# Kernel optimization log

Hardware: AMD Instinct MI355X
Metric: run time of the kernel (lower is better)

Reference implementation:

```python
import jax, jax.numpy as jnp
import numpy as np

B, S1, T = 32, 128, 50
E, H, L, V = 768, 1024, 3, 32000


def setup_inputs() -> dict:
    key = jax.random.key(0)
    ks = jax.random.split(key, 32)
    s = 0.02
    inp = {
        "x": jax.random.normal(ks[0], (B, S1, E), jnp.float32),
        "target_seq": jax.random.randint(ks[1], (B, T), 0, V),
        "emb": jax.random.normal(ks[2], (V, E), jnp.float32) * s,
        "attn_W1": jax.random.normal(ks[3], (H, E + H), jnp.float32) * s,
        "attn_b1": jnp.zeros((H,), jnp.float32),
        "attn_W2": jax.random.normal(ks[4], (1, H), jnp.float32) * s,
        "attn_b2": jnp.zeros((1,), jnp.float32),
        "fc_W": jax.random.normal(ks[5], (V, H), jnp.float32) * s,
        "fc_b": jnp.zeros((V,), jnp.float32),
    }
    for l in range(L):
        in_dim = 2 * E if l == 0 else H
        inp[f"Wih{l}"] = jax.random.normal(ks[6 + 4 * l], (4 * H, in_dim), jnp.float32) * s
        inp[f"Whh{l}"] = jax.random.normal(ks[7 + 4 * l], (4 * H, H), jnp.float32) * s
        inp[f"bih{l}"] = jnp.zeros((4 * H,), jnp.float32)
        inp[f"bhh{l}"] = jnp.zeros((4 * H,), jnp.float32)
    return inp


def _forward(x, target_seq, emb, attn_W1, attn_b1, attn_W2, attn_b2,
             Wih0, Whh0, bih0, bhh0, Wih1, Whh1, bih1, bhh1,
             Wih2, Whh2, bih2, bhh2, fc_W, fc_b):
    Bb, S, Edim = x.shape
    Hd = Whh0.shape[1]
    W1x, W1h = attn_W1[:, :Edim], attn_W1[:, Edim:]
    # precompute encoder-side part of the additive attention MLP: (B, S, H)
    xW = jnp.einsum('bse,he->bsh', x, W1x)
    emb_in = emb[target_seq]  # teacher forcing inputs (B, T, E)
    Wihs = (Wih0, Wih1, Wih2)
    Whhs = (Whh0, Whh1, Whh2)
    bihs = (bih0, bih1, bih2)
    bhhs = (bhh0, bhh1, bhh2)

    def step(carry, cur_in):
        h, c = carry  # each (L, B, H)
        hid = jax.nn.relu(xW + (h[-1] @ W1h.T)[:, None, :] + attn_b1)  # (B,S,H)
        scores = hid @ attn_W2[0] + attn_b2[0]  # (B, S)
        # NOTE: original module multiplies LOG-softmax weights by x (faithful)
        logw = jax.nn.log_softmax(scores, axis=1)[:, :, None]
        context = jnp.sum(logw * x, axis=1)  # (B, E)
        inp = jnp.concatenate([cur_in, context], axis=1)  # (B, 2E)
        new_h, new_c = [], []
        for l in range(3):
            gates = inp @ Wihs[l].T + h[l] @ Whhs[l].T + bihs[l] + bhhs[l]
            i, f, g, o = jnp.split(gates, 4, axis=1)  # torch gate order i,f,g,o
            cl = jax.nn.sigmoid(f) * c[l] + jax.nn.sigmoid(i) * jnp.tanh(g)
            hl = jax.nn.sigmoid(o) * jnp.tanh(cl)
            new_h.append(hl)
            new_c.append(cl)
            inp = hl
        h = jnp.stack(new_h)
        c = jnp.stack(new_c)
        logits = inp @ fc_W.T + fc_b  # (B, V)
        return (h, c), jax.nn.log_softmax(logits, axis=1)

    h0 = jnp.zeros((3, Bb, Hd), x.dtype)
    c0 = jnp.zeros_like(h0)
    _, outs = jax.lax.scan(step, (h0, c0), jnp.swapaxes(emb_in, 0, 1))
    return jnp.swapaxes(outs, 0, 1)  # (B, T, V)


def reference(x, target_seq, emb, attn_W1, attn_b1, attn_W2, attn_b2,
              Wih0, Whh0, bih0, bhh0, Wih1, Whh1, bih1, bhh1,
              Wih2, Whh2, bih2, bhh2, fc_W, fc_b):
    return _forward(x, target_seq, emb, attn_W1, attn_b1, attn_W2, attn_b2,
                    Wih0, Whh0, bih0, bhh0, Wih1, Whh1, bih1, bhh1,
                    Wih2, Whh2, bih2, bhh2, fc_W, fc_b)
```

## Files before the change

### kernel.cpp

```cpp
#include <hip/hip_runtime.h>
#include <math.h>

#define Bdim 32
#define Sdim 128
#define Tdim 50
#define Edim 768
#define Hdim 1024
#define Vdim 32000
#define EH   1792
#define INPD 1536
#define FCB  500

typedef __bf16 bf16x8 __attribute__((ext_vector_type(8)));
typedef float  f32x4  __attribute__((ext_vector_type(4)));

__device__ __forceinline__ float sigmf(float v){ return 1.0f / (1.0f + expf(-v)); }

__device__ __forceinline__ ushort f2b(float v){
  unsigned int b = __float_as_uint(v);
  unsigned int r = (b + 0x7fffu + ((b >> 16) & 1u)) >> 16;
  return (ushort)r;
}
__device__ __forceinline__ float b2f(ushort u){
  return __uint_as_float(((unsigned int)u) << 16);
}

__global__ __launch_bounds__(256) void cvt_bf16(const float* __restrict__ src,
                                                ushort* __restrict__ dst, int n4){
  int i = blockIdx.x * 256 + threadIdx.x;
  if (i >= n4) return;
  float4 v = *(const float4*)(src + (size_t)i * 4);
  *(ushort4*)(dst + (size_t)i * 4) = make_ushort4(f2b(v.x), f2b(v.y), f2b(v.z), f2b(v.w));
}

__global__ __launch_bounds__(256) void cvt_w1h(const float* __restrict__ aW1,
                                               ushort* __restrict__ dst){
  int i = blockIdx.x * 256 + threadIdx.x;
  if (i >= 262144) return;
  int k = (i & 255) * 4;
  int j = i >> 8;
  float4 v = *(const float4*)(aW1 + (size_t)j * EH + Edim + k);
  *(ushort4*)(dst + (size_t)j * 1024 + k) = make_ushort4(f2b(v.x), f2b(v.y), f2b(v.z), f2b(v.w));
}

__global__ __launch_bounds__(256) void zero_kernel(float* __restrict__ p, int n){
  int i = blockIdx.x * 256 + threadIdx.x;
  if (i < n) p[i] = 0.0f;
}

__global__ __launch_bounds__(256) void gather_emb_p(const int* __restrict__ tseq,
                                                    const float* __restrict__ emb,
                                                    ushort* __restrict__ inpP){
  int g = blockIdx.x * 256 + threadIdx.x;
  if (g >= Tdim * Bdim * 96) return;
  int kb = g % 96;
  int r = g / 96;
  int b = r % Bdim;
  int t = r / Bdim;
  int tok = tseq[b * Tdim + t];
  const float* src = emb + (size_t)tok * Edim + kb * 8;
  float4 a = *(const float4*)src;
  float4 c = *(const float4*)(src + 4);
  ushort* dst = inpP + (size_t)t * 49152 + kb * 256 + b * 8;
  *(ushort4*)(dst)     = make_ushort4(f2b(a.x), f2b(a.y), f2b(a.z), f2b(a.w));
  *(ushort4*)(dst + 4) = make_ushort4(f2b(c.x), f2b(c.y), f2b(c.z), f2b(c.w));
}

__global__ __launch_bounds__(256) void xw_gemm(const float* __restrict__ x,
                                               const float* __restrict__ w1,
                                               ushort* __restrict__ xWb){
  __shared__ float As[16][68];
  __shared__ float Ws[16][68];
  int tid = threadIdx.x;
  int m0 = blockIdx.x * 64;
  int n0 = blockIdx.y * 64;
  int lm = tid >> 2;
  int lk = (tid & 3) << 2;
  int tm = (tid >> 4) << 2;
  int tn = (tid & 15) << 2;
  float acc[4][4] = {};
  for (int k0 = 0; k0 < Edim; k0 += 16){
    float4 av = *(const float4*)&x [(size_t)(m0 + lm) * Edim + k0 + lk];
    float4 wv = *(const float4*)&w1[(size_t)(n0 + lm) * EH   + k0 + lk];
    As[lk+0][lm] = av.x; As[lk+1][lm] = av.y; As[lk+2][lm] = av.z; As[lk+3][lm] = av.w;
    Ws[lk+0][lm] = wv.x; Ws[lk+1][lm] = wv.y; Ws[lk+2][lm] = wv.z; Ws[lk+3][lm] = wv.w;
    __syncthreads();
#pragma unroll
    for (int k = 0; k < 16; k++){
      float a0 = As[k][tm+0], a1 = As[k][tm+1], a2 = As[k][tm+2], a3 = As[k][tm+3];
      float b0 = Ws[k][tn+0], b1 = Ws[k][tn+1], b2 = Ws[k][tn+2], b3 = Ws[k][tn+3];
      acc[0][0] += a0*b0; acc[0][1] += a0*b1; acc[0][2] += a0*b2; acc[0][3] += a0*b3;
      acc[1][0] += a1*b0; acc[1][1] += a1*b1; acc[1][2] += a1*b2; acc[1][3] += a1*b3;
      acc[2][0] += a2*b0; acc[2][1] += a2*b1; acc[2][2] += a2*b2; acc[2][3] += a2*b3;
      acc[3][0] += a3*b0; acc[3][1] += a3*b1; acc[3][2] += a3*b2; acc[3][3] += a3*b3;
    }
    __syncthreads();
  }
#pragma unroll
  for (int i = 0; i < 4; i++)
#pragma unroll
    for (int j = 0; j < 4; j++)
      xWb[(size_t)(m0 + tm + i) * Hdim + n0 + tn + j] = f2b(acc[i][j]);
}

template<bool ABF16>
__device__ __forceinline__ void mfma_tile(const void* A, int lda, int r,
                                          const ushort* __restrict__ Bp,
                                          int kbeg, int klen, int lane,
                                          f32x4& acc0, f32x4& acc1){
  int q = lane >> 4;
  const ushort* Ab = (const ushort*)A;
  const float*  Af = (const float*)A;
#pragma unroll 4
  for (int kk = kbeg; kk < kbeg + klen; kk += 32){
    bf16x8 a;
    if (ABF16){
      a = *reinterpret_cast<const bf16x8*>(Ab + (size_t)r * lda + kk + q * 8);
    } else {
      const float* p = Af + (size_t)r * lda + kk + q * 8;
      float4 u = *(const float4*)p;
      float4 w = *(const float4*)(p + 4);
      union { ushort s[8]; bf16x8 v; } t;
      t.s[0]=f2b(u.x); t.s[1]=f2b(u.y); t.s[2]=f2b(u.z); t.s[3]=f2b(u.w);
      t.s[4]=f2b(w.x); t.s[5]=f2b(w.y); t.s[6]=f2b(w.z); t.s[7]=f2b(w.w);
      a = t.v;
    }
    const ushort* bbase = Bp + ((kk >> 3) + q) * 256 + (lane & 15) * 8;
    bf16x8 b0 = *reinterpret_cast<const bf16x8*>(bbase);
    bf16x8 b1 = *reinterpret_cast<const bf16x8*>(bbase + 128);
    acc0 = __builtin_amdgcn_mfma_f32_16x16x32_bf16(a, b0, acc0, 0, 0, 0);
    acc1 = __builtin_amdgcn_mfma_f32_16x16x32_bf16(a, b1, acc1, 0, 0, 0);
  }
}

template<bool ABF16>
__global__ __launch_bounds__(256) void lstm_layer(const void* __restrict__ Wih, int Kin,
                                                  const void* __restrict__ Whh,
                                                  const ushort* __restrict__ inpP,
                                                  const ushort* __restrict__ hP,
                                                  const float* __restrict__ bih,
                                                  const float* __restrict__ bhh,
                                                  const float* __restrict__ cold,
                                                  float* __restrict__ cnew,
                                                  ushort* __restrict__ hPack){
  __shared__ float ld[4][4][4][32];
  int tid = threadIdx.x;
  int lane = tid & 63, kq = tid >> 6;
  int j0 = blockIdx.x * 4;
  int r = ((lane & 15) >> 2) * 1024 + j0 + (lane & 3);
  f32x4 acc0 = {0,0,0,0}, acc1 = {0,0,0,0};
  int kin_q = Kin >> 2;
  mfma_tile<ABF16>(Wih, Kin, r, inpP, kq * kin_q, kin_q, lane, acc0, acc1);
  mfma_tile<ABF16>(Whh, Hdim, r, hP, kq * 256, 256, lane, acc0, acc1);
  int g = lane >> 4, c = lane & 15;
#pragma unroll
  for (int rr = 0; rr < 4; rr++){
    ld[kq][g][rr][c]      = acc0[rr];
    ld[kq][g][rr][c + 16] = acc1[rr];
  }
  __syncthreads();
  if (tid < 128){
    int b = tid & 31, ul = tid >> 5;
    int j = j0 + ul;
    float gi = 0, gf = 0, gg = 0, go = 0;
#pragma unroll
    for (int k = 0; k < 4; k++){
      gi += ld[k][0][ul][b];
      gf += ld[k][1][ul][b];
      gg += ld[k][2][ul][b];
      go += ld[k][3][ul][b];
    }
    gi += bih[j]        + bhh[j];
    gf += bih[j + 1024] + bhh[j + 1024];
    gg += bih[j + 2048] + bhh[j + 2048];
    go += bih[j + 3072] + bhh[j + 3072];
    float cv = sigmf(gf) * cold[j * 32 + b] + sigmf(gi) * tanhf(gg);
    float hv = sigmf(go) * tanhf(cv);
    cnew[j * 32 + b] = cv;
    hPack[(j >> 3) * 256 + b * 8 + (j & 7)] = f2b(hv);
  }
}

__global__ __launch_bounds__(256) void attn_a_gemm(const ushort* __restrict__ W1h,
                                                   const ushort* __restrict__ h2P,
                                                   const float* __restrict__ b1,
                                                   float* __restrict__ aBuf){
  __shared__ float ld[4][32][17];
  int tid = threadIdx.x;
  int lane = tid & 63, kq = tid >> 6;
  int rowBase = blockIdx.x * 16;
  int r = rowBase + (lane & 15);
  f32x4 acc0 = {0,0,0,0}, acc1 = {0,0,0,0};
  mfma_tile<true>(W1h, Hdim, r, h2P, kq * 256, 256, lane, acc0, acc1);
  int q = lane >> 4, c = lane & 15;
#pragma unroll
  for (int rr = 0; rr < 4; rr++){
    ld[kq][c][q * 4 + rr]      = acc0[rr];
    ld[kq][c + 16][q * 4 + rr] = acc1[rr];
  }
  __syncthreads();
  int b = tid & 31, jl = tid >> 5;
#pragma unroll
  for (int h = 0; h < 2; h++){
    int j2 = jl + h * 8;
    float v = ld[0][b][j2] + ld[1][b][j2] + ld[2][b][j2] + ld[3][b][j2];
    int j = rowBase + j2;
    aBuf[b * 1024 + j] = v + b1[j];
  }
}

__global__ __launch_bounds__(256) void attn_score(const float* __restrict__ aBuf,
                                                  const float* __restrict__ w2,
                                                  const float* __restrict__ b2p,
                                                  const ushort* __restrict__ xWb,
                                                  float* __restrict__ scBuf){
  int b = blockIdx.x >> 2, sg = blockIdx.x & 3;
  int w = threadIdx.x >> 6, lane = threadIdx.x & 63;
  int jb = lane * 16;
  float ab[16], wv[16];
#pragma unroll
  for (int i = 0; i < 4; i++){
    *(float4*)&ab[i * 4] = *(const float4*)&aBuf[b * 1024 + jb + i * 4];
    *(float4*)&wv[i * 4] = *(const float4*)&w2[jb + i * 4];
  }
  float b2v = b2p[0];
#pragma unroll
  for (int si = 0; si < 8; si++){
    int s = sg * 32 + w * 8 + si;
    const ushort* xrow = xWb + (size_t)(b * Sdim + s) * Hdim + jb;
    bf16x8 x0 = *reinterpret_cast<const bf16x8*>(xrow);
    bf16x8 x1 = *reinterpret_cast<const bf16x8*>(xrow + 8);
    float acc = 0.0f;
#pragma unroll
    for (int i = 0; i < 8; i++){
      float h0 = fmaxf((float)x0[i] + ab[i], 0.0f);
      float h1 = fmaxf((float)x1[i] + ab[i + 8], 0.0f);
      acc += h0 * wv[i] + h1 * wv[i + 8];
    }
    for (int off = 32; off; off >>= 1) acc += __shfl_xor(acc, off);
    if (lane == 0) scBuf[b * Sdim + s] = acc + b2v;
  }
}

__global__ __launch_bounds__(256) void attn_ctx2(const float* __restrict__ scBuf,
                                                 const ushort* __restrict__ xbf,
                                                 ushort* __restrict__ inpPt){
  __shared__ float sb[Sdim];
  int b = blockIdx.x / 3, ec = blockIdx.x % 3;
  int tid = threadIdx.x;
  if (tid < Sdim) sb[tid] = scBuf[b * Sdim + tid];
  __syncthreads();
  if (tid < 64){
    float v0 = sb[tid], v1 = sb[tid + 64];
    float m = fmaxf(v0, v1);
    for (int off = 32; off; off >>= 1) m = fmaxf(m, __shfl_xor(m, off));
    float e = expf(v0 - m) + expf(v1 - m);
    for (int off = 32; off; off >>= 1) e += __shfl_xor(e, off);
    float lse = m + logf(e);
    sb[tid]      = v0 - lse;
    sb[tid + 64] = v1 - lse;
  }
  __syncthreads();
  int e = ec * 256 + tid;
  const ushort* xb = xbf + (size_t)b * Sdim * Edim + e;
  float acc = 0.0f;
#pragma unroll 8
  for (int s = 0; s < Sdim; s++) acc += sb[s] * b2f(xb[(size_t)s * Edim]);
  int k = Edim + e;
  inpPt[(k >> 3) * 256 + b * 8 + (k & 7)] = f2b(acc);
}

template<bool ABF16>
__global__ __launch_bounds__(512) void fc_gemm(const void* __restrict__ fcW,
                                               const ushort* __restrict__ hP,
                                               const float* __restrict__ fcb,
                                               float* __restrict__ logits,
                                               float* __restrict__ partM,
                                               float* __restrict__ partS){
  __shared__ float ld[2][32][73];
  int tid = threadIdx.x;
  int lane = tid & 63, w = tid >> 6;
  int khalf = w >> 2;
  int v0 = blockIdx.x * 64 + (w & 3) * 16;
  int r = v0 + (lane & 15);
  f32x4 acc0 = {0,0,0,0}, acc1 = {0,0,0,0};
  mfma_tile<ABF16>(fcW, Hdim, r, hP, khalf * 512, 512, lane, acc0, acc1);
  int q = lane >> 4, c = lane & 15;
#pragma unroll
  for (int rr = 0; rr < 4; rr++){
    int vloc = (w & 3) * 16 + q * 4 + rr;
    ld[khalf][c][vloc]      = acc0[rr];
    ld[khalf][c + 16][vloc] = acc1[rr];
  }
  __syncthreads();
  int b = tid >> 4, i0 = (tid & 15) * 4;
  int vg = blockIdx.x * 64 + i0;
  float o0 = ld[0][b][i0+0] + ld[1][b][i0+0] + fcb[vg+0];
  float o1 = ld[0][b][i0+1] + ld[1][b][i0+1] + fcb[vg+1];
  float o2 = ld[0][b][i0+2] + ld[1][b][i0+2] + fcb[vg+2];
  float o3 = ld[0][b][i0+3] + ld[1][b][i0+3] + fcb[vg+3];
  *(float4*)&logits[(size_t)b * Vdim + vg] = make_float4(o0, o1, o2, o3);
  float m = fmaxf(fmaxf(o0, o1), fmaxf(o2, o3));
  float s = expf(o0 - m) + expf(o1 - m) + expf(o2 - m) + expf(o3 - m);
#pragma unroll
  for (int off = 1; off < 16; off <<= 1){
    float m2 = __shfl_xor(m, off);
    float s2 = __shfl_xor(s, off);
    float nm = fmaxf(m, m2);
    s = s * expf(m - nm) + s2 * expf(m2 - nm);
    m = nm;
  }
  if ((tid & 15) == 0){
    partM[b * FCB + blockIdx.x] = m;
    partS[b * FCB + blockIdx.x] = s;
  }
}

__global__ __launch_bounds__(256) void lsm_write(const float* __restrict__ logits,
                                                 const float* __restrict__ partM,
                                                 const float* __restrict__ partS,
                                                 float* __restrict__ out, int t){
  __shared__ float sm[256], ss[256];
  int b = blockIdx.x, chunk = blockIdx.y;
  int tid = threadIdx.x;
  float m = -1e30f, s = 0.0f;
  for (int i = tid; i < FCB; i += 256){
    float m2 = partM[b * FCB + i];
    float s2 = partS[b * FCB + i];
    float nm = fmaxf(m, m2);
    s = s * expf(m - nm) + s2 * expf(m2 - nm);
    m = nm;
  }
  sm[tid] = m; ss[tid] = s;
  __syncthreads();
  for (int r = 128; r; r >>= 1){
    if (tid < r){
      float m2 = sm[tid + r], s2 = ss[tid + r];
      float nm = fmaxf(sm[tid], m2);
      ss[tid] = ss[tid] * expf(sm[tid] - nm) + s2 * expf(m2 - nm);
      sm[tid] = nm;
    }
    __syncthreads();
  }
  float lse = sm[0] + logf(ss[0]);
  if (tid < 250){
    int i4 = chunk * 250 + tid;
    float4 v = ((const float4*)logits)[(size_t)b * 8000 + i4];
    float4* dst = (float4*)(out + ((size_t)b * Tdim + t) * Vdim);
    dst[i4] = make_float4(v.x - lse, v.y - lse, v.z - lse, v.w - lse);
  }
}

extern "C" void kernel_launch(void* const* d_in, const int* in_sizes, int n_in,
                              void* d_out, int out_size, void* d_ws, size_t ws_size,
                              hipStream_t stream){
  const float* x    = (const float*)d_in[0];
  const int*   tseq = (const int*)  d_in[1];
  const float* emb  = (const float*)d_in[2];
  const float* aW1  = (const float*)d_in[3];
  const float* ab1  = (const float*)d_in[4];
  const float* aW2  = (const float*)d_in[5];
  const float* ab2  = (const float*)d_in[6];
  const float* fcW  = (const float*)d_in[7];
  const float* fcb  = (const float*)d_in[8];
  const float* Wih[3] = {(const float*)d_in[9],  (const float*)d_in[13], (const float*)d_in[17]};
  const float* Whh[3] = {(const float*)d_in[10], (const float*)d_in[14], (const float*)d_in[18]};
  const float* bih[3] = {(const float*)d_in[11], (const float*)d_in[15], (const float*)d_in[19]};
  const float* bhh[3] = {(const float*)d_in[12], (const float*)d_in[16], (const float*)d_in[20]};
  float* out = (float*)d_out;

  char* p = (char*)d_ws;
  ushort* xW_bf  = (ushort*)p;            p += (size_t)4096 * 1024 * 2;
  ushort* W1h_bf = (ushort*)p;            p += (size_t)1024 * 1024 * 2;
  ushort* inpP   = (ushort*)p;            p += (size_t)Tdim * 49152 * 2;
  ushort* x_bf   = (ushort*)p;            p += (size_t)Bdim * Sdim * Edim * 2;
  float*  aBuf   = (float*)p;             p += (size_t)Bdim * Hdim * 4;
  float*  scBuf  = (float*)p;             p += (size_t)Bdim * Sdim * 4;
  float*  partM  = (float*)p;             p += (size_t)Bdim * FCB * 4;
  float*  partS  = (float*)p;             p += (size_t)Bdim * FCB * 4;
  float*  logits = (float*)p;             p += (size_t)Bdim * Vdim * 4;
  float*  cBuf   = (float*)p;             p += (size_t)6 * 32768 * 4;
  ushort* hPackB = (ushort*)p;            p += (size_t)6 * 32768 * 2;
  ushort* fcW_bf  = (ushort*)p;           p += (size_t)Vdim * Hdim * 2;
  ushort* Wih_bf[3]; ushort* Whh_bf[3];
  Wih_bf[0] = (ushort*)p;                 p += (size_t)4096 * 1536 * 2;
  Whh_bf[0] = (ushort*)p;                 p += (size_t)4096 * 1024 * 2;
  Wih_bf[1] = (ushort*)p;                 p += (size_t)4096 * 1024 * 2;
  Whh_bf[1] = (ushort*)p;                 p += (size_t)4096 * 1024 * 2;
  Wih_bf[2] = (ushort*)p;                 p += (size_t)4096 * 1024 * 2;
  Whh_bf[2] = (ushort*)p;                 p += (size_t)4096 * 1024 * 2;
  size_t need_full = (size_t)(p - (char*)d_ws);
  bool full = ws_size >= need_full;

  zero_kernel<<<(294912 + 255) / 256, 256, 0, stream>>>(cBuf, 294912);
  gather_emb_p<<<(Tdim * Bdim * 96 + 255) / 256, 256, 0, stream>>>(tseq, emb, inpP);
  cvt_w1h<<<262144 / 256, 256, 0, stream>>>(aW1, W1h_bf);
  cvt_bf16<<<(Bdim * Sdim * Edim / 4 + 255) / 256, 256, 0, stream>>>(x, x_bf, Bdim * Sdim * Edim / 4);
  xw_gemm<<<dim3(64, 16), 256, 0, stream>>>(x, aW1, xW_bf);
  if (full){
    cvt_bf16<<<(Vdim * Hdim / 4 + 255) / 256, 256, 0, stream>>>(fcW, fcW_bf, Vdim * Hdim / 4);
    cvt_bf16<<<(4096 * 1536 / 4 + 255) / 256, 256, 0, stream>>>(Wih[0], Wih_bf[0], 4096 * 1536 / 4);
    cvt_bf16<<<(4096 * 1024 / 4 + 255) / 256, 256, 0, stream>>>(Whh[0], Whh_bf[0], 4096 * 1024 / 4);
    cvt_bf16<<<(4096 * 1024 / 4 + 255) / 256, 256, 0, stream>>>(Wih[1], Wih_bf[1], 4096 * 1024 / 4);
    cvt_bf16<<<(4096 * 1024 / 4 + 255) / 256, 256, 0, stream>>>(Whh[1], Whh_bf[1], 4096 * 1024 / 4);
    cvt_bf16<<<(4096 * 1024 / 4 + 255) / 256, 256, 0, stream>>>(Wih[2], Wih_bf[2], 4096 * 1024 / 4);
    cvt_bf16<<<(4096 * 1024 / 4 + 255) / 256, 256, 0, stream>>>(Whh[2], Whh_bf[2], 4096 * 1024 / 4);
  }

  #define HP(l, par)  (hPackB + ((l) * 2 + (par)) * 32768)
  #define CB(l, par)  (cBuf   + ((l) * 2 + (par)) * 32768)

  for (int t = 0; t < Tdim; t++){
    int pn = t & 1, po = 1 - pn;
    ushort* inpPt = inpP + (size_t)t * 49152;

    attn_a_gemm<<<64, 256, 0, stream>>>(W1h_bf, HP(2, po), ab1, aBuf);
    attn_score<<<128, 256, 0, stream>>>(aBuf, aW2, ab2, xW_bf, scBuf);
    attn_ctx2<<<96, 256, 0, stream>>>(scBuf, x_bf, inpPt);

    for (int l = 0; l < 3; l++){
      const ushort* bin = (l == 0) ? inpPt : HP(l - 1, pn);
      int kin = (l == 0) ? INPD : Hdim;
      if (full)
        lstm_layer<true ><<<256, 256, 0, stream>>>(Wih_bf[l], kin, Whh_bf[l], bin, HP(l, po),
                                                   bih[l], bhh[l], CB(l, po), CB(l, pn), HP(l, pn));
      else
        lstm_layer<false><<<256, 256, 0, stream>>>(Wih[l],    kin, Whh[l],    bin, HP(l, po),
                                                   bih[l], bhh[l], CB(l, po), CB(l, pn), HP(l, pn));
    }

    if (full) fc_gemm<true ><<<FCB, 512, 0, stream>>>(fcW_bf, HP(2, pn), fcb, logits, partM, partS);
    else      fc_gemm<false><<<FCB, 512, 0, stream>>>(fcW,    HP(2, pn), fcb, logits, partM, partS);
    lsm_write<<<dim3(Bdim, 32), 256, 0, stream>>>(logits, partM, partS, out, t);
  }
}
```

Before: 4.001 ms.

## Fuse all decoder timesteps into one persistent kernel with grid barriers

```diff
diff --git a/kernel.cpp b/kernel.cpp
--- a/kernel.cpp
+++ b/kernel.cpp
@@ -10,6 +10,8 @@
 #define EH   1792
 #define INPD 1536
 #define FCB  500
+#define FCB2 250
+#define NBLK 256
 
 typedef __bf16 bf16x8 __attribute__((ext_vector_type(8)));
 typedef float  f32x4  __attribute__((ext_vector_type(4)));
@@ -101,6 +103,28 @@
 #pragma unroll
     for (int j = 0; j < 4; j++)
       xWb[(size_t)(m0 + tm + i) * Hdim + n0 + tn + j] = f2b(acc[i][j]);
+}
+
+__global__ __launch_bounds__(256) void xpose_x(const ushort* __restrict__ xbf,
+                                               ushort* __restrict__ xT){
+  __shared__ ushort tl[64][132];
+  int b  = blockIdx.x / 12;
+  int et = blockIdx.x % 12;
+  int e0 = et * 64;
+  int el = threadIdx.x & 63;
+  int s4 = threadIdx.x >> 6;
+#pragma unroll
+  for (int s0 = 0; s0 < Sdim; s0 += 4){
+    int s = s0 + s4;
+    tl[el][s] = xbf[((size_t)(b * Sdim + s)) * Edim + e0 + el];
+  }
+  __syncthreads();
+  int e  = threadIdx.x >> 2;
+  int sc = (threadIdx.x & 3) * 32;
+  ushort* dst = xT + ((size_t)b * Edim + e0 + e) * Sdim + sc;
+#pragma unroll
+  for (int i = 0; i < 4; i++)
+    *(ushort4*)(dst + i * 8) = *(ushort4*)&tl[e][sc + i * 8];
 }
 
 template<bool ABF16>
@@ -351,6 +375,275 @@
   }
 }
 
+struct PArgs {
+  const ushort *W1h, *xW, *xT, *fcWb;
+  const ushort *Wih0, *Whh0, *Wih1, *Whh1, *Wih2, *Whh2;
+  ushort *inpP, *hPackB;
+  const float *ab1, *aW2, *ab2, *fcb;
+  const float *bih0, *bhh0, *bih1, *bhh1, *bih2, *bhh2;
+  float *aBuf, *partM, *partS, *logits, *cBuf, *out;
+  unsigned *bar;
+};
+
+union ShU {
+  float a8[8][32][17];
+  float sb[Sdim];
+  float ll[8][4][4][32];
+  float fc[32][132];
+  struct { float sm[512]; float ss[512]; } g;
+};
+
+__device__ __forceinline__ void gridbar(unsigned* bar){
+  __syncthreads();
+  if (threadIdx.x == 0){
+    __threadfence();
+    unsigned* gp = bar + 576;
+    unsigned g = __hip_atomic_load(gp, __ATOMIC_RELAXED, __HIP_MEMORY_SCOPE_AGENT);
+    unsigned* cnt = bar + (blockIdx.x & 7) * 64;
+    unsigned a = __hip_atomic_fetch_add(cnt, 1u, __ATOMIC_RELAXED, __HIP_MEMORY_SCOPE_AGENT);
+    if (a == 31u){
+      __hip_atomic_store(cnt, 0u, __ATOMIC_RELAXED, __HIP_MEMORY_SCOPE_AGENT);
+      __threadfence();
+      unsigned r = __hip_atomic_fetch_add(bar + 512, 1u, __ATOMIC_RELAXED, __HIP_MEMORY_SCOPE_AGENT);
+      if (r == 7u){
+        __hip_atomic_store(bar + 512, 0u, __ATOMIC_RELAXED, __HIP_MEMORY_SCOPE_AGENT);
+        __threadfence();
+        __hip_atomic_store(gp, g + 1u, __ATOMIC_RELAXED, __HIP_MEMORY_SCOPE_AGENT);
+      }
+    }
+    int guard = 0;
+    while (__hip_atomic_load(gp, __ATOMIC_RELAXED, __HIP_MEMORY_SCOPE_AGENT) == g){
+      __builtin_amdgcn_s_sleep(2);
+      if (++guard > 300000) break;
+    }
+    __threadfence();
+  }
+  __syncthreads();
+}
+
+__device__ __forceinline__ void lstm_stage(ShU& sh, const ushort* Wih, int Kin,
+                                           const ushort* Whh, const ushort* bin,
+                                           const ushort* hOld,
+                                           const float* bihL, const float* bhhL,
+                                           const float* cOld, float* cNew,
+                                           ushort* hNew, int tid, int lane, int wid,
+                                           int blk){
+  int j0 = blk * 4;
+  int r = ((lane & 15) >> 2) * 1024 + j0 + (lane & 3);
+  f32x4 acc0 = {0,0,0,0}, acc1 = {0,0,0,0};
+  int ke = Kin >> 3;
+  mfma_tile<true>(Wih, Kin, r, bin, wid * ke, ke, lane, acc0, acc1);
+  mfma_tile<true>(Whh, Hdim, r, hOld, wid * 128, 128, lane, acc0, acc1);
+  int g = lane >> 4, c = lane & 15;
+#pragma unroll
+  for (int rr = 0; rr < 4; rr++){
+    sh.ll[wid][g][rr][c]      = acc0[rr];
+    sh.ll[wid][g][rr][c + 16] = acc1[rr];
+  }
+  __syncthreads();
+  if (tid < 128){
+    int b = tid & 31, ul = tid >> 5;
+    int j = j0 + ul;
+    float gi = 0, gf = 0, gg = 0, go = 0;
+#pragma unroll
+    for (int k = 0; k < 8; k++){
+      gi += sh.ll[k][0][ul][b];
+      gf += sh.ll[k][1][ul][b];
+      gg += sh.ll[k][2][ul][b];
+      go += sh.ll[k][3][ul][b];
+    }
+    gi += bihL[j]        + bhhL[j];
+    gf += bihL[j + 1024] + bhhL[j + 1024];
+    gg += bihL[j + 2048] + bhhL[j + 2048];
+    go += bihL[j + 3072] + bhhL[j + 3072];
+    float cv = sigmf(gf) * cOld[j * 32 + b] + sigmf(gi) * tanhf(gg);
+    float hv = sigmf(go) * tanhf(cv);
+    cNew[j * 32 + b] = cv;
+    hNew[(j >> 3) * 256 + b * 8 + (j & 7)] = f2b(hv);
+  }
+}
+
+__global__ __launch_bounds__(512, 2) void persistent_all(PArgs p){
+  extern __shared__ char smem[];
+  ShU& sh = *reinterpret_cast<ShU*>(smem);
+  int tid  = threadIdx.x;
+  int blk  = blockIdx.x;
+  int lane = tid & 63;
+  int wid  = tid >> 6;
+
+  for (int t = 0; t < Tdim; t++){
+    int pn = t & 1, po = 1 - pn;
+    ushort* inpPt = p.inpP + (size_t)t * 49152;
+    const ushort* h2old = p.hPackB + (size_t)(2 * 2 + po) * 32768;
+
+    if (blk < 64){
+      int rowBase = blk * 16;
+      int r = rowBase + (lane & 15);
+      f32x4 acc0 = {0,0,0,0}, acc1 = {0,0,0,0};
+      mfma_tile<true>(p.W1h, Hdim, r, h2old, wid * 128, 128, lane, acc0, acc1);
+      int q = lane >> 4, c = lane & 15;
+#pragma unroll
+      for (int rr = 0; rr < 4; rr++){
+        sh.a8[wid][c][q * 4 + rr]      = acc0[rr];
+        sh.a8[wid][c + 16][q * 4 + rr] = acc1[rr];
+      }
+      __syncthreads();
+      int b = tid & 31, jl = tid >> 5;
+      float v = 0;
+#pragma unroll
+      for (int k = 0; k < 8; k++) v += sh.a8[k][b][jl];
+      int j = rowBase + jl;
+      p.aBuf[b * 1024 + j] = v + p.ab1[j];
+    }
+    gridbar(p.bar);
+
+    if (blk < 32){
+      int b = blk;
+      int jb = lane * 16;
+      float ab[16], w2r[16];
+#pragma unroll
+      for (int i = 0; i < 4; i++){
+        *(float4*)&ab[i * 4]  = *(const float4*)&p.aBuf[b * 1024 + jb + i * 4];
+        *(float4*)&w2r[i * 4] = *(const float4*)&p.aW2[jb + i * 4];
+      }
+      float b2v = p.ab2[0];
+#pragma unroll 2
+      for (int si = 0; si < 16; si++){
+        int s = wid * 16 + si;
+        const ushort* xrow = p.xW + (size_t)(b * Sdim + s) * Hdim + jb;
+        bf16x8 x0 = *reinterpret_cast<const bf16x8*>(xrow);
+        bf16x8 x1 = *reinterpret_cast<const bf16x8*>(xrow + 8);
+        float acc = 0.0f;
+#pragma unroll
+        for (int i = 0; i < 8; i++){
+          float h0 = fmaxf((float)x0[i] + ab[i], 0.0f);
+          float h1 = fmaxf((float)x1[i] + ab[i + 8], 0.0f);
+          acc += h0 * w2r[i] + h1 * w2r[i + 8];
+        }
+        for (int off = 32; off; off >>= 1) acc += __shfl_xor(acc, off);
+        if (lane == 0) sh.sb[s] = acc + b2v;
+      }
+      __syncthreads();
+      if (tid < 64){
+        float v0 = sh.sb[tid], v1 = sh.sb[tid + 64];
+        float m = fmaxf(v0, v1);
+        for (int off = 32; off; off >>= 1) m = fmaxf(m, __shfl_xor(m, off));
+        float e = expf(v0 - m) + expf(v1 - m);
+        for (int off = 32; off; off >>= 1) e += __shfl_xor(e, off);
+        float lse = m + logf(e);
+        sh.sb[tid]      = v0 - lse;
+        sh.sb[tid + 64] = v1 - lse;
+      }
+      __syncthreads();
+#pragma unroll
+      for (int half = 0; half < 2; half++){
+        int e = half * 512 + tid;
+        if (e < Edim){
+          const ushort* xr = p.xT + ((size_t)b * Edim + e) * Sdim;
+          float acc = 0.0f;
+#pragma unroll
+          for (int s8 = 0; s8 < 16; s8++){
+            bf16x8 xv = *reinterpret_cast<const bf16x8*>(xr + s8 * 8);
+#pragma unroll
+            for (int k = 0; k < 8; k++) acc += sh.sb[s8 * 8 + k] * (float)xv[k];
+          }
+          int kk = Edim + e;
+          inpPt[(kk >> 3) * 256 + b * 8 + (kk & 7)] = f2b(acc);
+        }
+      }
+    }
+    gridbar(p.bar);
+
+    {
+      ushort* hb = p.hPackB;  float* cb = p.cBuf;
+      lstm_stage(sh, p.Wih0, INPD, p.Whh0, inpPt,
+                 hb + (0 * 2 + po) * 32768, p.bih0, p.bhh0,
+                 cb + (0 * 2 + po) * 32768, cb + (0 * 2 + pn) * 32768,
+                 hb + (0 * 2 + pn) * 32768, tid, lane, wid, blk);
+      gridbar(p.bar);
+      lstm_stage(sh, p.Wih1, Hdim, p.Whh1, hb + (0 * 2 + pn) * 32768,
+                 hb + (1 * 2 + po) * 32768, p.bih1, p.bhh1,
+                 cb + (1 * 2 + po) * 32768, cb + (1 * 2 + pn) * 32768,
+                 hb + (1 * 2 + pn) * 32768, tid, lane, wid, blk);
+      gridbar(p.bar);
+      lstm_stage(sh, p.Wih2, Hdim, p.Whh2, hb + (1 * 2 + pn) * 32768,
+                 hb + (2 * 2 + po) * 32768, p.bih2, p.bhh2,
+                 cb + (2 * 2 + po) * 32768, cb + (2 * 2 + pn) * 32768,
+                 hb + (2 * 2 + pn) * 32768, tid, lane, wid, blk);
+      gridbar(p.bar);
+    }
+
+    if (blk < FCB2){
+      const ushort* h2new = p.hPackB + (size_t)(2 * 2 + pn) * 32768;
+      int v0 = blk * 128 + wid * 16;
+      int r = v0 + (lane & 15);
+      f32x4 acc0 = {0,0,0,0}, acc1 = {0,0,0,0};
+      mfma_tile<true>(p.fcWb, Hdim, r, h2new, 0, Hdim, lane, acc0, acc1);
+      int q = lane >> 4, c = lane & 15;
+#pragma unroll
+      for (int rr = 0; rr < 4; rr++){
+        sh.fc[c][wid * 16 + q * 4 + rr]      = acc0[rr];
+        sh.fc[c + 16][wid * 16 + q * 4 + rr] = acc1[rr];
+      }
+      __syncthreads();
+      int b = tid >> 4, i0 = (tid & 15) * 8;
+      int vg = blk * 128 + i0;
+      float o[8];
+#pragma unroll
+      for (int j = 0; j < 8; j++) o[j] = sh.fc[b][i0 + j] + p.fcb[vg + j];
+      *(float4*)&p.logits[(size_t)b * Vdim + vg]     = make_float4(o[0], o[1], o[2], o[3]);
+      *(float4*)&p.logits[(size_t)b * Vdim + vg + 4] = make_float4(o[4], o[5], o[6], o[7]);
+      float m = o[0];
+#pragma unroll
+      for (int j = 1; j < 8; j++) m = fmaxf(m, o[j]);
+      float s = 0.0f;
+#pragma unroll
+      for (int j = 0; j < 8; j++) s += expf(o[j] - m);
+#pragma unroll
+      for (int off = 1; off < 16; off <<= 1){
+        float m2 = __shfl_xor(m, off);
+        float s2 = __shfl_xor(s, off);
+        float nm = fmaxf(m, m2);
+        s = s * expf(m - nm) + s2 * expf(m2 - nm);
+        m = nm;
+      }
+      if ((tid & 15) == 0){
+        p.partM[b * FCB2 + blk] = m;
+        p.partS[b * FCB2 + blk] = s;
+      }
+    }
+    gridbar(p.bar);
+
+    {
+      int b = blk >> 3, chunk = blk & 7;
+      float m = -1e30f, s = 0.0f;
+      if (tid < FCB2){ m = p.partM[b * FCB2 + tid]; s = p.partS[b * FCB2 + tid]; }
+      sh.g.sm[tid] = m; sh.g.ss[tid] = s;
+      __syncthreads();
+      for (int rr = 256; rr > 0; rr >>= 1){
+        if (tid < rr){
+          float m2 = sh.g.sm[tid + rr], s2 = sh.g.ss[tid + rr];
+          float nm = fmaxf(sh.g.sm[tid], m2);
+          sh.g.ss[tid] = sh.g.ss[tid] * expf(sh.g.sm[tid] - nm) + s2 * expf(m2 - nm);
+          sh.g.sm[tid] = nm;
+        }
+        __syncthreads();
+      }
+      float lse = sh.g.sm[0] + logf(sh.g.ss[0]);
+      const float4* lg = (const float4*)(p.logits + (size_t)b * Vdim);
+      float4* dst = (float4*)(p.out + ((size_t)b * Tdim + t) * Vdim);
+#pragma unroll
+      for (int it = 0; it < 2; it++){
+        int i4 = chunk * 1000 + it * 512 + tid;
+        if (i4 < chunk * 1000 + 1000){
+          float4 v = lg[i4];
+          dst[i4] = make_float4(v.x - lse, v.y - lse, v.z - lse, v.w - lse);
+        }
+      }
+    }
+  }
+}
+
 extern "C" void kernel_launch(void* const* d_in, const int* in_sizes, int n_in,
                               void* d_out, int out_size, void* d_ws, size_t ws_size,
                               hipStream_t stream){
@@ -381,6 +674,7 @@
   float*  logits = (float*)p;             p += (size_t)Bdim * Vdim * 4;
   float*  cBuf   = (float*)p;             p += (size_t)6 * 32768 * 4;
   ushort* hPackB = (ushort*)p;            p += (size_t)6 * 32768 * 2;
+  unsigned* barBuf = (unsigned*)p;        p += (size_t)1024 * 4;
   ushort* fcW_bf  = (ushort*)p;           p += (size_t)Vdim * Hdim * 2;
   ushort* Wih_bf[3]; ushort* Whh_bf[3];
   Wih_bf[0] = (ushort*)p;                 p += (size_t)4096 * 1536 * 2;
@@ -389,15 +683,17 @@
   Whh_bf[1] = (ushort*)p;                 p += (size_t)4096 * 1024 * 2;
   Wih_bf[2] = (ushort*)p;                 p += (size_t)4096 * 1024 * 2;
   Whh_bf[2] = (ushort*)p;                 p += (size_t)4096 * 1024 * 2;
+  ushort* xT_bf = (ushort*)p;             p += (size_t)Bdim * Edim * Sdim * 2;
   size_t need_full = (size_t)(p - (char*)d_ws);
   bool full = ws_size >= need_full;
 
-  zero_kernel<<<(294912 + 255) / 256, 256, 0, stream>>>(cBuf, 294912);
+  zero_kernel<<<(295936 + 255) / 256, 256, 0, stream>>>(cBuf, 295936);
   gather_emb_p<<<(Tdim * Bdim * 96 + 255) / 256, 256, 0, stream>>>(tseq, emb, inpP);
   cvt_w1h<<<262144 / 256, 256, 0, stream>>>(aW1, W1h_bf);
   cvt_bf16<<<(Bdim * Sdim * Edim / 4 + 255) / 256, 256, 0, stream>>>(x, x_bf, Bdim * Sdim * Edim / 4);
   xw_gemm<<<dim3(64, 16), 256, 0, stream>>>(x, aW1, xW_bf);
   if (full){
+    xpose_x<<<Bdim * 12, 256, 0, stream>>>(x_bf, xT_bf);
     cvt_bf16<<<(Vdim * Hdim / 4 + 255) / 256, 256, 0, stream>>>(fcW, fcW_bf, Vdim * Hdim / 4);
     cvt_bf16<<<(4096 * 1536 / 4 + 255) / 256, 256, 0, stream>>>(Wih[0], Wih_bf[0], 4096 * 1536 / 4);
     cvt_bf16<<<(4096 * 1024 / 4 + 255) / 256, 256, 0, stream>>>(Whh[0], Whh_bf[0], 4096 * 1024 / 4);
@@ -405,6 +701,24 @@
     cvt_bf16<<<(4096 * 1024 / 4 + 255) / 256, 256, 0, stream>>>(Whh[1], Whh_bf[1], 4096 * 1024 / 4);
     cvt_bf16<<<(4096 * 1024 / 4 + 255) / 256, 256, 0, stream>>>(Wih[2], Wih_bf[2], 4096 * 1024 / 4);
     cvt_bf16<<<(4096 * 1024 / 4 + 255) / 256, 256, 0, stream>>>(Whh[2], Whh_bf[2], 4096 * 1024 / 4);
+
+    hipFuncSetAttribute(reinterpret_cast<const void*>(persistent_all),
+                        hipFuncAttributeMaxDynamicSharedMemorySize, 86016);
+    PArgs pa;
+    pa.W1h = W1h_bf; pa.xW = xW_bf; pa.xT = xT_bf; pa.fcWb = fcW_bf;
+    pa.Wih0 = Wih_bf[0]; pa.Whh0 = Whh_bf[0];
+    pa.Wih1 = Wih_bf[1]; pa.Whh1 = Whh_bf[1];
+    pa.Wih2 = Wih_bf[2]; pa.Whh2 = Whh_bf[2];
+    pa.inpP = inpP; pa.hPackB = hPackB;
+    pa.ab1 = ab1; pa.aW2 = aW2; pa.ab2 = ab2; pa.fcb = fcb;
+    pa.bih0 = bih[0]; pa.bhh0 = bhh[0];
+    pa.bih1 = bih[1]; pa.bhh1 = bhh[1];
+    pa.bih2 = bih[2]; pa.bhh2 = bhh[2];
+    pa.aBuf = aBuf; pa.partM = partM; pa.partS = partS;
+    pa.logits = logits; pa.cBuf = cBuf; pa.out = out;
+    pa.bar = barBuf;
+    persistent_all<<<NBLK, 512, 86016, stream>>>(pa);
+    return;
   }
 
   #define HP(l, par)  (hPackB + ((l) * 2 + (par)) * 32768)
@@ -421,16 +735,11 @@
     for (int l = 0; l < 3; l++){
       const ushort* bin = (l == 0) ? inpPt : HP(l - 1, pn);
       int kin = (l == 0) ? INPD : Hdim;
-      if (full)
-        lstm_layer<true ><<<256, 256, 0, stream>>>(Wih_bf[l], kin, Whh_bf[l], bin, HP(l, po),
-                                                   bih[l], bhh[l], CB(l, po), CB(l, pn), HP(l, pn));
-      else
-        lstm_layer<false><<<256, 256, 0, stream>>>(Wih[l],    kin, Whh[l],    bin, HP(l, po),
-                                                   bih[l], bhh[l], CB(l, po), CB(l, pn), HP(l, pn));
-    }
-
-    if (full) fc_gemm<true ><<<FCB, 512, 0, stream>>>(fcW_bf, HP(2, pn), fcb, logits, partM, partS);
-    else      fc_gemm<false><<<FCB, 512, 0, stream>>>(fcW,    HP(2, pn), fcb, logits, partM, partS);
+      lstm_layer<false><<<256, 256, 0, stream>>>(Wih[l], kin, Whh[l], bin, HP(l, po),
+                                                 bih[l], bhh[l], CB(l, po), CB(l, pn), HP(l, pn));
+    }
+
+    fc_gemm<false><<<FCB, 512, 0, stream>>>(fcW, HP(2, pn), fcb, logits, partM, partS);
     lsm_write<<<dim3(Bdim, 32), 256, 0, stream>>>(logits, partM, partS, out, t);
   }
 }
```

New measurement: 6.785 ms. +69.6%, slower.
